# Kernel tuning notes

Hardware: AMD Instinct MI355X
Metric: run time of the kernel (lower is better)

## Reference

```python
import jax, jax.numpy as jnp
import numpy as np

N, E = 50000, 800000
IN_FEAT = OUT_FEAT = 128
EMB = 3
K = 3  # k_order + 1
BN_EPS = 1e-5


def setup_inputs() -> dict:
    key = jax.random.key(0)
    ks = jax.random.split(key, 12)
    feature = jax.random.normal(ks[0], (N, IN_FEAT), jnp.float32)
    coords = jax.random.normal(ks[1], (N, EMB), jnp.float32)
    src = jax.random.randint(ks[2], (E,), 0, N, jnp.int32)
    dst = jax.random.randint(ks[3], (E,), 0, N, jnp.int32)
    order = jax.random.randint(ks[4], (E,), 0, K, jnp.int32)
    # xavier_normal_ on [K, in, out]: torch treats last two dims as (fan_in, fan_out)
    std_lin = float(np.sqrt(2.0 / (IN_FEAT + OUT_FEAT)))
    linear = jax.random.normal(ks[5], (K, IN_FEAT, OUT_FEAT), jnp.float32) * std_lin
    # attention_layer: Linear(EMB, OUT_FEAT, bias=False); store as [EMB, OUT_FEAT]
    lim_att = float(1.0 / np.sqrt(EMB))
    attW = jax.random.uniform(ks[6], (EMB, OUT_FEAT), jnp.float32, -lim_att, lim_att)
    lim_mlp = float(1.0 / np.sqrt(OUT_FEAT))
    mlp_w = jax.random.uniform(ks[7], (OUT_FEAT, OUT_FEAT), jnp.float32, -lim_mlp, lim_mlp)
    mlp_b = jax.random.uniform(ks[8], (OUT_FEAT,), jnp.float32, -lim_mlp, lim_mlp)
    bn_gamma = jnp.ones((OUT_FEAT,), jnp.float32)
    bn_beta = jnp.zeros((OUT_FEAT,), jnp.float32)
    return {"feature": feature, "coords": coords, "src": src, "dst": dst,
            "order": order, "linear": linear, "attW": attW,
            "mlp_w": mlp_w, "mlp_b": mlp_b, "bn_gamma": bn_gamma, "bn_beta": bn_beta}


def reference(feature, coords, src, dst, order, linear, attW, mlp_w, mlp_b, bn_gamma, bn_beta):
    n = feature.shape[0]
    # --- edge attention: dot(attention_layer(c_src - c_dst), h_src) ---
    dc = coords[src] - coords[dst]                      # [E, EMB]
    att = jnp.sum((dc @ attW) * feature[src], axis=1)   # [E]
    invdist = 1.0 / (jnp.sum(dc * dc, axis=1) + 1.0)    # [E], 1/(||dc||^2 + 1)
    # --- messages: per-edge weight selection linear[order] @ h_src ---
    # msg depends only on (src node, order): precompute per-order node transforms
    xk = jnp.einsum('ni,kio->kno', feature, linear)     # [K, N, OUT]
    msg = xk[order, src]                                # [E, OUT]
    # --- segment softmax over incoming edges of dst ---
    m = jax.ops.segment_max(att, dst, num_segments=n)   # [N]
    ex = jnp.exp(att - m[dst])                          # [E]
    denom = jax.ops.segment_sum(ex, dst, num_segments=n)
    d_g = denom[dst]
    alpha = ex / jnp.where(d_g > 0, d_g, 1.0)
    # --- weighted scatter-add aggregation ---
    w = (alpha * invdist)[:, None]                      # [E, 1]
    h = jax.ops.segment_sum(w * msg, dst, num_segments=n)  # [N, OUT]
    # --- mlp: Linear -> ReLU -> BatchNorm1d (training-mode batch stats) ---
    y = jax.nn.relu(h @ mlp_w.T + mlp_b)
    mean = jnp.mean(y, axis=0)
    var = jnp.var(y, axis=0)  # biased, matches torch BN normalization
    y = (y - mean) * jax.lax.rsqrt(var + BN_EPS) * bn_gamma + bn_beta
    return y
```

## Files before the change

### kernel.cpp

```cpp
#include <hip/hip_runtime.h>

#define N_NODES 50000
#define E_EDGES 800000
#define FEAT    128
#define KORD    3
#define BN_EPS  1e-5f
#define NBUK    49
#define BCAP    20480
#define NSHARD  16
#define NSEG    128
#define NGC_BLKS 3125
#define NWB_BLKS 12500
#define NZERO   4352

typedef __fp16 f16x2 __attribute__((ext_vector_type(2)));
typedef __fp16 f16x8 __attribute__((ext_vector_type(8)));
typedef __attribute__((ext_vector_type(4))) float f32x4;

__device__ __forceinline__ unsigned h2u(f16x2 h) { union { f16x2 h; unsigned u; } c; c.h = h; return c.u; }
__device__ __forceinline__ f16x2 u2h(unsigned u) { union { unsigned u; f16x2 h; } c; c.u = u; return c.h; }

__device__ __forceinline__ void gload16(const void* g, void* l) {
    __builtin_amdgcn_global_load_lds(
        (const __attribute__((address_space(1))) unsigned int*)g,
        (__attribute__((address_space(3))) unsigned int*)l, 16, 0, 0);
}

__global__ void g_cast(const float* __restrict__ feat,
                       const float* __restrict__ coords,
                       const float* __restrict__ attW,
                       const float* __restrict__ W,
                       const float* __restrict__ L,
                       __fp16* __restrict__ fh,
                       float4* __restrict__ pk,
                       __fp16* __restrict__ GT,
                       int* __restrict__ zbase) {
    __shared__ float wrow[FEAT];
    const int gtid = blockIdx.x * 256 + threadIdx.x;
    if (gtid < NZERO) zbase[gtid] = 0;
    if (blockIdx.x >= NGC_BLKS) {
        const int o = blockIdx.x - NGC_BLKS;
        const int i = threadIdx.x;
        if (i < FEAT) wrow[i] = W[o * FEAT + i];
        __syncthreads();
        if (i < FEAT) {
            #pragma unroll
            for (int k = 0; k < KORD; ++k) {
                const float* lp = L + ((size_t)k * FEAT + i) * FEAT;
                float acc = 0.f;
                #pragma unroll 8
                for (int j = 0; j < FEAT; ++j) acc = fmaf(lp[j], wrow[j], acc);
                GT[(size_t)o * 384 + k * FEAT + i] = (__fp16)acc;
            }
        }
        return;
    }
    const int node = blockIdx.x * 16 + (threadIdx.x >> 4);
    const int sub  = threadIdx.x & 15;
    const float4 fa = *(const float4*)(feat + (size_t)node * FEAT + sub * 8);
    const float4 fb = *(const float4*)(feat + (size_t)node * FEAT + sub * 8 + 4);
    uint4 ov;
    ov.x = h2u(__builtin_amdgcn_cvt_pkrtz(fa.x, fa.y));
    ov.y = h2u(__builtin_amdgcn_cvt_pkrtz(fa.z, fa.w));
    ov.z = h2u(__builtin_amdgcn_cvt_pkrtz(fb.x, fb.y));
    ov.w = h2u(__builtin_amdgcn_cvt_pkrtz(fb.z, fb.w));
    *(uint4*)(fh + (size_t)node * FEAT + sub * 8) = ov;
    float g0, g1, g2;
    {
        const float4 wa0 = *(const float4*)(attW + 0 * FEAT + sub * 8);
        const float4 wb0 = *(const float4*)(attW + 0 * FEAT + sub * 8 + 4);
        const float4 wa1 = *(const float4*)(attW + 1 * FEAT + sub * 8);
        const float4 wb1 = *(const float4*)(attW + 1 * FEAT + sub * 8 + 4);
        const float4 wa2 = *(const float4*)(attW + 2 * FEAT + sub * 8);
        const float4 wb2 = *(const float4*)(attW + 2 * FEAT + sub * 8 + 4);
        g0 = fa.x*wa0.x + fa.y*wa0.y + fa.z*wa0.z + fa.w*wa0.w
           + fb.x*wb0.x + fb.y*wb0.y + fb.z*wb0.z + fb.w*wb0.w;
        g1 = fa.x*wa1.x + fa.y*wa1.y + fa.z*wa1.z + fa.w*wa1.w
           + fb.x*wb1.x + fb.y*wb1.y + fb.z*wb1.z + fb.w*wb1.w;
        g2 = fa.x*wa2.x + fa.y*wa2.y + fa.z*wa2.z + fa.w*wa2.w
           + fb.x*wb2.x + fb.y*wb2.y + fb.z*wb2.z + fb.w*wb2.w;
    }
    #pragma unroll
    for (int off = 8; off; off >>= 1) {
        g0 += __shfl_xor(g0, off);
        g1 += __shfl_xor(g1, off);
        g2 += __shfl_xor(g2, off);
    }
    if (sub == 0) {
        const float c0 = coords[node * 3 + 0], c1 = coords[node * 3 + 1], c2 = coords[node * 3 + 2];
        pk[2 * node]     = make_float4(c0, c1, c2, g0);
        pk[2 * node + 1] = make_float4(g1, g2, 0.f, 0.f);
    }
}

__global__ __launch_bounds__(256)
void bucketA(const int* __restrict__ src, const int* __restrict__ dst,
             const int* __restrict__ order,
             int* __restrict__ gcur, int2* __restrict__ bbuf) {
    __shared__ int lcnt[4][NBUK];
    __shared__ int wbase[4][NBUK];
    const int tid = threadIdx.x;
    const int wid = tid >> 6;
    if (tid < NBUK) {
        lcnt[0][tid] = 0; lcnt[1][tid] = 0; lcnt[2][tid] = 0; lcnt[3][tid] = 0;
    }
    __syncthreads();
    const int e0 = blockIdx.x * 2048;
    int b[8], r[8], so[8], dd[8];
    #pragma unroll
    for (int i = 0; i < 8; ++i) {
        const int e = e0 + i * 256 + tid;
        if (e < E_EDGES) {
            dd[i] = dst[e];
            so[i] = (order[e] << 16) | src[e];
            b[i] = dd[i] >> 10;
            r[i] = atomicAdd(&lcnt[wid][b[i]], 1);
        } else b[i] = -1;
    }
    __syncthreads();
    if (tid < NBUK) {
        const int w0 = lcnt[0][tid], w1 = lcnt[1][tid], w2 = lcnt[2][tid], w3 = lcnt[3][tid];
        const int base = atomicAdd(gcur + tid, w0 + w1 + w2 + w3);
        wbase[0][tid] = base;
        wbase[1][tid] = base + w0;
        wbase[2][tid] = base + w0 + w1;
        wbase[3][tid] = base + w0 + w1 + w2;
    }
    __syncthreads();
    #pragma unroll
    for (int i = 0; i < 8; ++i)
        if (b[i] >= 0)
            bbuf[(size_t)b[i] * BCAP + wbase[wid][b[i]] + r[i]] = make_int2(so[i], dd[i]);
}

__global__ __launch_bounds__(256)
void hist2(const int* __restrict__ gcur, const int2* __restrict__ bbuf,
           int* __restrict__ rowptr, int* __restrict__ cursor) {
    __shared__ int lhist[1024];
    __shared__ int lscan[256];
    __shared__ int boff_s;
    const int b = blockIdx.x;
    const int t = threadIdx.x;
    #pragma unroll
    for (int i = 0; i < 4; ++i) lhist[t + i * 256] = 0;
    __syncthreads();
    const int n = gcur[b];
    const int base = b << 10;
    for (int i = t; i < n; i += 256)
        atomicAdd(&lhist[bbuf[(size_t)b * BCAP + i].y - base], 1);
    __syncthreads();
    if (t < 64) {
        const int v = (t < NBUK) ? gcur[t] : 0;
        int incl = v;
        #pragma unroll
        for (int off = 1; off < 64; off <<= 1) {
            const int u = __shfl_up(incl, off);
            if (t >= off) incl += u;
        }
        if (t == b) boff_s = incl - v;
    }
    int v[4];
    #pragma unroll
    for (int i = 0; i < 4; ++i) v[i] = lhist[t * 4 + i];
    lscan[t] = v[0] + v[1] + v[2] + v[3];
    __syncthreads();
    for (int off = 1; off < 256; off <<= 1) {
        const int u = (t >= off) ? lscan[t - off] : 0;
        __syncthreads();
        lscan[t] += u;
        __syncthreads();
    }
    int excl = (t ? lscan[t - 1] : 0) + boff_s;
    #pragma unroll
    for (int i = 0; i < 4; ++i) {
        const int node = base + t * 4 + i;
        if (node < N_NODES) { rowptr[node] = excl; cursor[node] = excl; }
        excl += v[i];
    }
    if (b == 0 && t == 0) rowptr[N_NODES] = E_EDGES;
}

__global__ void bucketB(const int* __restrict__ gcur, const int2* __restrict__ bbuf,
                        const float4* __restrict__ pk,
                        int* __restrict__ cursor, int4* __restrict__ edata) {
    const int b = blockIdx.x / NSEG;
    const int seg = blockIdx.x % NSEG;
    const int n = gcur[b];
    const int lo = (int)((long)n * seg / NSEG), hi = (int)((long)n * (seg + 1) / NSEG);
    for (int i = lo + (int)threadIdx.x; i < hi; i += 256) {
        const int2 ent = bbuf[(size_t)b * BCAP + i];
        const int s = ent.x & 0xFFFF;
        const int d = ent.y;
        const float4 a0 = pk[2 * s], a1 = pk[2 * s + 1], c0 = pk[2 * d];
        const float dx = a0.x - c0.x, dy = a0.y - c0.y, dz = a0.z - c0.z;
        const float att  = dx * a0.w + dy * a1.x + dz * a1.y;
        const float invd = 1.f / (dx * dx + dy * dy + dz * dz + 1.f);
        const int pos = atomicAdd(cursor + d, 1);
        edata[pos] = make_int4(ent.x, __float_as_int(att), __float_as_int(invd), 0);
    }
}

__global__ void segagg(const int4* __restrict__ edata,
                       const int* __restrict__ rowptr,
                       const __fp16* __restrict__ fh,
                       __fp16* __restrict__ agg) {
    __shared__ uint4 stash[4][64];
    const int node = (blockIdx.x * blockDim.x + threadIdx.x) >> 6;
    const int lane = threadIdx.x & 63;
    const int wid  = threadIdx.x >> 6;
    if (node >= N_NODES) return;
    const int beg = rowptr[node], end = rowptr[node + 1];

    int4 e0c = make_int4(0, 0xFF800000, 0, 0);
    float m = -1e30f, s = 0.f;
    int nch = 0;
    for (int cb = beg; cb < end; cb += 64, ++nch) {
        const int p = cb + lane;
        float a = -1e30f;
        if (p < end) {
            const int4 e = edata[p];
            a = __int_as_float(e.y);
            if (nch == 0) e0c = e;
        }
        const float mn = fmaxf(m, a);
        s = s * __expf(m - mn) + ((p < end) ? __expf(a - mn) : 0.f);
        m = mn;
    }
    #pragma unroll
    for (int off = 32; off; off >>= 1) {
        const float mo = __shfl_xor(m, off), so_ = __shfl_xor(s, off);
        const float mn = fmaxf(m, mo);
        s = s * __expf(m - mn) + so_ * __expf(mo - mn);
        m = mn;
    }
    const float inv_s = s > 0.f ? 1.f / s : 0.f;

    const int grp = lane >> 4;
    const int fl  = lane & 15;
    f16x2 ac[3][4];
    #pragma unroll
    for (int o = 0; o < 3; ++o)
        #pragma unroll
        for (int q = 0; q < 4; ++q) ac[o][q] = (f16x2){0, 0};

    int ch = 0;
    for (int cb = beg; cb < end; cb += 64, ++ch) {
        const int p = cb + lane;
        float wl = 0.f; int so = 0;
        if (p < end) {
            const int4 e = (ch == 0) ? e0c : edata[p];
            wl = __expf(__int_as_float(e.y) - m) * inv_s * __int_as_float(e.z);
            so = e.x;
        }
        const int k = so >> 16;
        const __fp16 wh = (__fp16)wl;
        f16x2 w2; w2.x = wh; w2.y = wh;
        const unsigned uw = h2u(w2);
        stash[wid][lane] = make_uint4(k == 0 ? uw : 0u, k == 1 ? uw : 0u,
                                      k == 2 ? uw : 0u, (unsigned)(so & 0xFFFF));
        const int ne = min(64, end - cb);
        const uint4* st = stash[wid];
        for (int t = 0; t < ne; t += 8) {
            const uint4 e1 = st[t + grp];
            const uint4 e2 = st[t + 4 + grp];
            const uint4 v1 = *(const uint4*)(fh + ((size_t)e1.w << 7) + fl * 8);
            const uint4 v2 = *(const uint4*)(fh + ((size_t)e2.w << 7) + fl * 8);
            {
                const f16x2 w0 = u2h(e1.x), w1 = u2h(e1.y), w2v = u2h(e1.z);
                const f16x2 va = u2h(v1.x), vb = u2h(v1.y), vc = u2h(v1.z), vd = u2h(v1.w);
                ac[0][0] = __builtin_elementwise_fma(va, w0, ac[0][0]);
                ac[0][1] = __builtin_elementwise_fma(vb, w0, ac[0][1]);
                ac[0][2] = __builtin_elementwise_fma(vc, w0, ac[0][2]);
                ac[0][3] = __builtin_elementwise_fma(vd, w0, ac[0][3]);
                ac[1][0] = __builtin_elementwise_fma(va, w1, ac[1][0]);
                ac[1][1] = __builtin_elementwise_fma(vb, w1, ac[1][1]);
                ac[1][2] = __builtin_elementwise_fma(vc, w1, ac[1][2]);
                ac[1][3] = __builtin_elementwise_fma(vd, w1, ac[1][3]);
                ac[2][0] = __builtin_elementwise_fma(va, w2v, ac[2][0]);
                ac[2][1] = __builtin_elementwise_fma(vb, w2v, ac[2][1]);
                ac[2][2] = __builtin_elementwise_fma(vc, w2v, ac[2][2]);
                ac[2][3] = __builtin_elementwise_fma(vd, w2v, ac[2][3]);
            }
            {
                const f16x2 w0 = u2h(e2.x), w1 = u2h(e2.y), w2v = u2h(e2.z);
                const f16x2 va = u2h(v2.x), vb = u2h(v2.y), vc = u2h(v2.z), vd = u2h(v2.w);
                ac[0][0] = __builtin_elementwise_fma(va, w0, ac[0][0]);
                ac[0][1] = __builtin_elementwise_fma(vb, w0, ac[0][1]);
                ac[0][2] = __builtin_elementwise_fma(vc, w0, ac[0][2]);
                ac[0][3] = __builtin_elementwise_fma(vd, w0, ac[0][3]);
                ac[1][0] = __builtin_elementwise_fma(va, w1, ac[1][0]);
                ac[1][1] = __builtin_elementwise_fma(vb, w1, ac[1][1]);
                ac[1][2] = __builtin_elementwise_fma(vc, w1, ac[1][2]);
                ac[1][3] = __builtin_elementwise_fma(vd, w1, ac[1][3]);
                ac[2][0] = __builtin_elementwise_fma(va, w2v, ac[2][0]);
                ac[2][1] = __builtin_elementwise_fma(vb, w2v, ac[2][1]);
                ac[2][2] = __builtin_elementwise_fma(vc, w2v, ac[2][2]);
                ac[2][3] = __builtin_elementwise_fma(vd, w2v, ac[2][3]);
            }
        }
    }
    #pragma unroll
    for (int o = 0; o < 3; ++o)
        #pragma unroll
        for (int q = 0; q < 4; ++q) {
            ac[o][q] = ac[o][q] + u2h(__shfl_xor((int)h2u(ac[o][q]), 16));
            ac[o][q] = ac[o][q] + u2h(__shfl_xor((int)h2u(ac[o][q]), 32));
        }
    if (lane < 16) {
        __fp16* row = agg + (size_t)node * 384 + fl * 8;
        *(uint4*)(row)       = make_uint4(h2u(ac[0][0]), h2u(ac[0][1]), h2u(ac[0][2]), h2u(ac[0][3]));
        *(uint4*)(row + 128) = make_uint4(h2u(ac[1][0]), h2u(ac[1][1]), h2u(ac[1][2]), h2u(ac[1][3]));
        *(uint4*)(row + 256) = make_uint4(h2u(ac[2][0]), h2u(ac[2][1]), h2u(ac[2][2]), h2u(ac[2][3]));
    }
}

__global__ __launch_bounds__(256)
void mlp_gemm(const __fp16* __restrict__ agg, const __fp16* __restrict__ GT,
              float* __restrict__ out, int M,
              const float* __restrict__ bias, float* __restrict__ sbuf) {
    __shared__ char smem[49152];
    const int m0 = blockIdx.x * 64;
    const int tid = threadIdx.x;
    const int wave = tid >> 6, lane = tid & 63;
    const int wm0 = wave * 16;
    const int lrow = lane & 15;
    const int kg = lane >> 4;
    const int srow = lane >> 3;
    const int schunk = lane & 7;

    auto STAGE = [&](int buf, int kc) {
        char* base = smem + buf * 24576;
        #pragma unroll
        for (int j = 0; j < 2; ++j) {
            const int rl = wave * 16 + j * 8 + srow;
            const int rg = min(m0 + rl, M - 1);
            gload16(agg + (size_t)rg * 384 + kc * 64 + ((schunk ^ (rl & 7)) << 3),
                    base + (wave * 16 + j * 8) * 128);
        }
        #pragma unroll
        for (int j = 0; j < 4; ++j) {
            const int rl = wave * 32 + j * 8 + srow;
            gload16(GT + (size_t)rl * 384 + kc * 64 + ((schunk ^ (rl & 7)) << 3),
                    base + 8192 + (wave * 32 + j * 8) * 128);
        }
    };

    f32x4 acc[8];
    #pragma unroll
    for (int b = 0; b < 8; ++b) acc[b] = (f32x4){0.f, 0.f, 0.f, 0.f};

    STAGE(0, 0);
    __syncthreads();

    for (int kc = 0; kc < 6; ++kc) {
        const int buf = kc & 1;
        if (kc < 5) STAGE(buf ^ 1, kc + 1);
        const char* Ab = smem + buf * 24576;
        const char* Bb = Ab + 8192;
        f16x8 afr[2];
        #pragma unroll
        for (int ks = 0; ks < 2; ++ks) {
            const int row = wm0 + lrow;
            afr[ks] = *(const f16x8*)(Ab + row * 128 + (((ks * 4 + kg) ^ (row & 7)) << 4));
        }
        #pragma unroll
        for (int nf = 0; nf < 8; ++nf) {
            #pragma unroll
            for (int ks = 0; ks < 2; ++ks) {
                const int row = nf * 16 + lrow;
                f16x8 bfr = *(const f16x8*)(Bb + row * 128 + (((ks * 4 + kg) ^ (row & 7)) << 4));
                acc[nf] = __builtin_amdgcn_mfma_f32_16x16x32_f16(afr[ks], bfr, acc[nf], 0, 0, 0);
            }
        }
        __syncthreads();
    }

    float s[8], s2[8], bv[8];
    #pragma unroll
    for (int nf = 0; nf < 8; ++nf) { s[nf] = 0.f; s2[nf] = 0.f; bv[nf] = bias[nf * 16 + lrow]; }
    #pragma unroll
    for (int nf = 0; nf < 8; ++nf)
        #pragma unroll
        for (int rg = 0; rg < 4; ++rg) {
            const int row = m0 + wm0 + kg * 4 + rg;
            if (row < M) {
                const float v = fmaxf(acc[nf][rg] + bv[nf], 0.f);
                out[(size_t)row * FEAT + nf * 16 + lrow] = v;
                s[nf] += v;
                s2[nf] = fmaf(v, v, s2[nf]);
            }
        }
    #pragma unroll
    for (int nf = 0; nf < 8; ++nf) {
        s[nf]  += __shfl_xor(s[nf], 16);  s[nf]  += __shfl_xor(s[nf], 32);
        s2[nf] += __shfl_xor(s2[nf], 16); s2[nf] += __shfl_xor(s2[nf], 32);
    }
    __syncthreads();
    float* red = (float*)smem;
    if (lane < 16) {
        #pragma unroll
        for (int nf = 0; nf < 8; ++nf) {
            red[wave * 256 + nf * 16 + lane]       = s[nf];
            red[wave * 256 + 128 + nf * 16 + lane] = s2[nf];
        }
    }
    __syncthreads();
    if (tid < 128) {
        const float ss = red[tid] + red[256 + tid] + red[512 + tid] + red[768 + tid];
        const float qq = red[128 + tid] + red[384 + tid] + red[640 + tid] + red[896 + tid];
        float* sb = sbuf + (blockIdx.x & (NSHARD - 1)) * 256;
        atomicAdd(sb + tid, ss);
        atomicAdd(sb + FEAT + tid, qq);
    }
}

__global__ void normalize(float* __restrict__ y, const float* __restrict__ sbuf,
                          const float* __restrict__ gamma, const float* __restrict__ beta) {
    __shared__ float sc_s[FEAT], sh_s[FEAT];
    const int t = threadIdx.x;
    if (t < FEAT) {
        float ssum = 0.f, qsum = 0.f;
        #pragma unroll
        for (int sh = 0; sh < NSHARD; ++sh) {
            ssum += sbuf[sh * 256 + t];
            qsum += sbuf[sh * 256 + 128 + t];
        }
        const float mean = ssum / (float)N_NODES;
        const float var  = qsum / (float)N_NODES - mean * mean;
        const float sc   = gamma[t] * rsqrtf(var + BN_EPS);
        sc_s[t] = sc;
        sh_s[t] = beta[t] - mean * sc;
    }
    __syncthreads();
    const int idx = blockIdx.x * blockDim.x + t;
    const int o4 = (idx & 31) * 4;
    float4 v = *(float4*)(y + (size_t)idx * 4);
    const float4 sc = *(const float4*)(sc_s + o4);
    const float4 sh = *(const float4*)(sh_s + o4);
    v.x = fmaf(v.x, sc.x, sh.x);
    v.y = fmaf(v.y, sc.y, sh.y);
    v.z = fmaf(v.z, sc.z, sh.z);
    v.w = fmaf(v.w, sc.w, sh.w);
    *(float4*)(y + (size_t)idx * 4) = v;
}

extern "C" void kernel_launch(void* const* d_in, const int* in_sizes, int n_in,
                              void* d_out, int out_size, void* d_ws, size_t ws_size,
                              hipStream_t stream) {
    const float* feature = (const float*)d_in[0];
    const float* coords  = (const float*)d_in[1];
    const int*   src     = (const int*)d_in[2];
    const int*   dst     = (const int*)d_in[3];
    const int*   order   = (const int*)d_in[4];
    const float* linear  = (const float*)d_in[5];
    const float* attW    = (const float*)d_in[6];
    const float* mlp_w   = (const float*)d_in[7];
    const float* mlp_b   = (const float*)d_in[8];
    const float* gamma   = (const float*)d_in[9];
    const float* beta    = (const float*)d_in[10];
    float* out = (float*)d_out;

    char* p = (char*)d_ws;
    __fp16* fh           = (__fp16*)p;  p += (size_t)N_NODES * FEAT * 2;
    __fp16* agg          = (__fp16*)p;  p += (size_t)N_NODES * 384 * 2;
    __fp16* GT           = (__fp16*)p;  p += (size_t)FEAT * 384 * 2;
    float4* pk           = (float4*)p;  p += (size_t)N_NODES * 32;
    int4*  edata         = (int4*)p;    p += (size_t)E_EDGES * 16;
    int2*  bbuf          = (int2*)p;    p += (size_t)NBUK * BCAP * 8;
    float* sbuf          = (float*)p;   p += NSHARD * 256 * 4;
    int*   gcur          = (int*)p;     p += 1024;
    int*   rowptr        = (int*)p;     p += 200064;
    int*   cursor        = (int*)p;     p += 200064;

    const int MB = (N_NODES + 63) / 64;
    const int AB = (E_EDGES + 2047) / 2048;

    g_cast<<<NGC_BLKS + FEAT, 256, 0, stream>>>(feature, coords, attW,
                                                mlp_w, linear, fh, pk, GT, (int*)sbuf);

    bucketA<<<AB, 256, 0, stream>>>(src, dst, order, gcur, bbuf);
    hist2<<<NBUK, 256, 0, stream>>>(gcur, bbuf, rowptr, cursor);
    bucketB<<<NBUK * NSEG, 256, 0, stream>>>(gcur, bbuf, pk, cursor, edata);

    segagg<<<NWB_BLKS, 256, 0, stream>>>(edata, rowptr, fh, agg);

    mlp_gemm<<<MB, 256, 0, stream>>>(agg, GT, out, N_NODES, mlp_b, sbuf);
    normalize<<<(N_NODES * 32) / 256, 256, 0, stream>>>(out, sbuf, gamma, beta);
}
```

Measured before the change: 151.6 us.

## Pack edge data to fp16, single-pass softmax for small degrees, fp16 MLP staging

Edge records shrink from 16 to 8 bytes by packing attention logit and inverse distance as fp16 pairs, which halves edge-buffer write and read traffic. Segment aggregation gets a fast path for nodes with at most 64 incoming edges: it loads edges once and reduces the max and sum across the wavefront, instead of making two passes. The MLP output is staged as fp16 in the reused feature buffer before normalization, so the intermediate write and read are smaller. The cost is lower precision in the attention logits and in the pre-BN activations.

```diff
diff --git a/kernel.cpp b/kernel.cpp
--- a/kernel.cpp
+++ b/kernel.cpp
@@ -182,7 +182,7 @@
 
 __global__ void bucketB(const int* __restrict__ gcur, const int2* __restrict__ bbuf,
                         const float4* __restrict__ pk,
-                        int* __restrict__ cursor, int4* __restrict__ edata) {
+                        int* __restrict__ cursor, int2* __restrict__ edata) {
     const int b = blockIdx.x / NSEG;
     const int seg = blockIdx.x % NSEG;
     const int n = gcur[b];
@@ -196,11 +196,11 @@
         const float att  = dx * a0.w + dy * a1.x + dz * a1.y;
         const float invd = 1.f / (dx * dx + dy * dy + dz * dz + 1.f);
         const int pos = atomicAdd(cursor + d, 1);
-        edata[pos] = make_int4(ent.x, __float_as_int(att), __float_as_int(invd), 0);
-    }
-}
-
-__global__ void segagg(const int4* __restrict__ edata,
+        edata[pos] = make_int2(ent.x, (int)h2u(__builtin_amdgcn_cvt_pkrtz(att, invd)));
+    }
+}
+
+__global__ void segagg(const int2* __restrict__ edata,
                        const int* __restrict__ rowptr,
                        const __fp16* __restrict__ fh,
                        __fp16* __restrict__ agg) {
@@ -210,30 +210,7 @@
     const int wid  = threadIdx.x >> 6;
     if (node >= N_NODES) return;
     const int beg = rowptr[node], end = rowptr[node + 1];
-
-    int4 e0c = make_int4(0, 0xFF800000, 0, 0);
-    float m = -1e30f, s = 0.f;
-    int nch = 0;
-    for (int cb = beg; cb < end; cb += 64, ++nch) {
-        const int p = cb + lane;
-        float a = -1e30f;
-        if (p < end) {
-            const int4 e = edata[p];
-            a = __int_as_float(e.y);
-            if (nch == 0) e0c = e;
-        }
-        const float mn = fmaxf(m, a);
-        s = s * __expf(m - mn) + ((p < end) ? __expf(a - mn) : 0.f);
-        m = mn;
-    }
-    #pragma unroll
-    for (int off = 32; off; off >>= 1) {
-        const float mo = __shfl_xor(m, off), so_ = __shfl_xor(s, off);
-        const float mn = fmaxf(m, mo);
-        s = s * __expf(m - mn) + so_ * __expf(mo - mn);
-        m = mn;
-    }
-    const float inv_s = s > 0.f ? 1.f / s : 0.f;
+    const int deg = end - beg;
 
     const int grp = lane >> 4;
     const int fl  = lane & 15;
@@ -243,22 +220,15 @@
         #pragma unroll
         for (int q = 0; q < 4; ++q) ac[o][q] = (f16x2){0, 0};
 
-    int ch = 0;
-    for (int cb = beg; cb < end; cb += 64, ++ch) {
-        const int p = cb + lane;
-        float wl = 0.f; int so = 0;
-        if (p < end) {
-            const int4 e = (ch == 0) ? e0c : edata[p];
-            wl = __expf(__int_as_float(e.y) - m) * inv_s * __int_as_float(e.z);
-            so = e.x;
-        }
+    auto STASH = [&](float wl, int so) {
         const int k = so >> 16;
         const __fp16 wh = (__fp16)wl;
         f16x2 w2; w2.x = wh; w2.y = wh;
         const unsigned uw = h2u(w2);
         stash[wid][lane] = make_uint4(k == 0 ? uw : 0u, k == 1 ? uw : 0u,
                                       k == 2 ? uw : 0u, (unsigned)(so & 0xFFFF));
-        const int ne = min(64, end - cb);
+    };
+    auto GATHER = [&](int ne) {
         const uint4* st = stash[wid];
         for (int t = 0; t < ne; t += 8) {
             const uint4 e1 = st[t + grp];
@@ -298,7 +268,59 @@
                 ac[2][3] = __builtin_elementwise_fma(vd, w2v, ac[2][3]);
             }
         }
-    }
+    };
+
+    if (deg <= 64) {
+        int so = 0; float a = -1e30f, iv = 0.f;
+        if (lane < deg) {
+            const int2 e = edata[beg + lane];
+            so = e.x;
+            const f16x2 ai = u2h((unsigned)e.y);
+            a  = (float)ai.x;
+            iv = (float)ai.y;
+        }
+        float m = a;
+        #pragma unroll
+        for (int off = 32; off; off >>= 1) m = fmaxf(m, __shfl_xor(m, off));
+        const float ex = (lane < deg) ? __expf(a - m) : 0.f;
+        float s = ex;
+        #pragma unroll
+        for (int off = 32; off; off >>= 1) s += __shfl_xor(s, off);
+        const float wl = ex * (s > 0.f ? 1.f / s : 0.f) * iv;
+        STASH(wl, so);
+        GATHER(deg);
+    } else {
+        float m = -1e30f, s = 0.f;
+        for (int cb = beg; cb < end; cb += 64) {
+            const int p = cb + lane;
+            float a = -1e30f;
+            if (p < end) a = (float)u2h((unsigned)edata[p].y).x;
+            const float mn = fmaxf(m, a);
+            s = s * __expf(m - mn) + ((p < end) ? __expf(a - mn) : 0.f);
+            m = mn;
+        }
+        #pragma unroll
+        for (int off = 32; off; off >>= 1) {
+            const float mo = __shfl_xor(m, off), so_ = __shfl_xor(s, off);
+            const float mn = fmaxf(m, mo);
+            s = s * __expf(m - mn) + so_ * __expf(mo - mn);
+            m = mn;
+        }
+        const float inv_s = s > 0.f ? 1.f / s : 0.f;
+        for (int cb = beg; cb < end; cb += 64) {
+            const int p = cb + lane;
+            float wl = 0.f; int so = 0;
+            if (p < end) {
+                const int2 e = edata[p];
+                so = e.x;
+                const f16x2 ai = u2h((unsigned)e.y);
+                wl = __expf((float)ai.x - m) * inv_s * (float)ai.y;
+            }
+            STASH(wl, so);
+            GATHER(min(64, end - cb));
+        }
+    }
+
     #pragma unroll
     for (int o = 0; o < 3; ++o)
         #pragma unroll
@@ -316,7 +338,7 @@
 
 __global__ __launch_bounds__(256)
 void mlp_gemm(const __fp16* __restrict__ agg, const __fp16* __restrict__ GT,
-              float* __restrict__ out, int M,
+              __fp16* __restrict__ yh, int M,
               const float* __restrict__ bias, float* __restrict__ sbuf) {
     __shared__ char smem[49152];
     const int m0 = blockIdx.x * 64;
@@ -385,7 +407,7 @@
             const int row = m0 + wm0 + kg * 4 + rg;
             if (row < M) {
                 const float v = fmaxf(acc[nf][rg] + bv[nf], 0.f);
-                out[(size_t)row * FEAT + nf * 16 + lrow] = v;
+                yh[(size_t)row * FEAT + nf * 16 + lrow] = (__fp16)v;
                 s[nf] += v;
                 s2[nf] = fmaf(v, v, s2[nf]);
             }
@@ -414,7 +436,8 @@
     }
 }
 
-__global__ void normalize(float* __restrict__ y, const float* __restrict__ sbuf,
+__global__ void normalize(const __fp16* __restrict__ yh, float* __restrict__ out,
+                          const float* __restrict__ sbuf,
                           const float* __restrict__ gamma, const float* __restrict__ beta) {
     __shared__ float sc_s[FEAT], sh_s[FEAT];
     const int t = threadIdx.x;
@@ -432,16 +455,21 @@
         sh_s[t] = beta[t] - mean * sc;
     }
     __syncthreads();
-    const int idx = blockIdx.x * blockDim.x + t;
-    const int o4 = (idx & 31) * 4;
-    float4 v = *(float4*)(y + (size_t)idx * 4);
-    const float4 sc = *(const float4*)(sc_s + o4);
-    const float4 sh = *(const float4*)(sh_s + o4);
-    v.x = fmaf(v.x, sc.x, sh.x);
-    v.y = fmaf(v.y, sc.y, sh.y);
-    v.z = fmaf(v.z, sc.z, sh.z);
-    v.w = fmaf(v.w, sc.w, sh.w);
-    *(float4*)(y + (size_t)idx * 4) = v;
+    const int idx = blockIdx.x * 256 + t;
+    const int f0 = (idx & 15) * 8;
+    const uint4 hv = *(const uint4*)(yh + (size_t)idx * 8);
+    const f16x2 h0 = u2h(hv.x), h1 = u2h(hv.y), h2v = u2h(hv.z), h3 = u2h(hv.w);
+    float4 o0, o1;
+    o0.x = fmaf((float)h0.x,  sc_s[f0 + 0], sh_s[f0 + 0]);
+    o0.y = fmaf((float)h0.y,  sc_s[f0 + 1], sh_s[f0 + 1]);
+    o0.z = fmaf((float)h1.x,  sc_s[f0 + 2], sh_s[f0 + 2]);
+    o0.w = fmaf((float)h1.y,  sc_s[f0 + 3], sh_s[f0 + 3]);
+    o1.x = fmaf((float)h2v.x, sc_s[f0 + 4], sh_s[f0 + 4]);
+    o1.y = fmaf((float)h2v.y, sc_s[f0 + 5], sh_s[f0 + 5]);
+    o1.z = fmaf((float)h3.x,  sc_s[f0 + 6], sh_s[f0 + 6]);
+    o1.w = fmaf((float)h3.y,  sc_s[f0 + 7], sh_s[f0 + 7]);
+    *(float4*)(out + (size_t)idx * 8)     = o0;
+    *(float4*)(out + (size_t)idx * 8 + 4) = o1;
 }
 
 extern "C" void kernel_launch(void* const* d_in, const int* in_sizes, int n_in,
@@ -465,7 +493,7 @@
     __fp16* agg          = (__fp16*)p;  p += (size_t)N_NODES * 384 * 2;
     __fp16* GT           = (__fp16*)p;  p += (size_t)FEAT * 384 * 2;
     float4* pk           = (float4*)p;  p += (size_t)N_NODES * 32;
-    int4*  edata         = (int4*)p;    p += (size_t)E_EDGES * 16;
+    int2*  edata         = (int2*)p;    p += (size_t)E_EDGES * 8;
     int2*  bbuf          = (int2*)p;    p += (size_t)NBUK * BCAP * 8;
     float* sbuf          = (float*)p;   p += NSHARD * 256 * 4;
     int*   gcur          = (int*)p;     p += 1024;
@@ -484,6 +512,6 @@
 
     segagg<<<NWB_BLKS, 256, 0, stream>>>(edata, rowptr, fh, agg);
 
-    mlp_gemm<<<MB, 256, 0, stream>>>(agg, GT, out, N_NODES, mlp_b, sbuf);
-    normalize<<<(N_NODES * 32) / 256, 256, 0, stream>>>(out, sbuf, gamma, beta);
-}
+    mlp_gemm<<<MB, 256, 0, stream>>>(agg, GT, fh , N_NODES, mlp_b, sbuf);
+    normalize<<<(N_NODES * FEAT / 8 + 255) / 256, 256, 0, stream>>>(fh, out, sbuf, gamma, beta);
+}
```

Result: no change. 152.0 us (+0.2%).
